# Optimization experiments

Measured on AMD Instinct MI355X. Metric: run time of the kernel, lower is better.

Reference implementation:

```python
import jax, jax.numpy as jnp
import numpy as np

SAMPLE_RATE = 44100
MAX_DURATION = 5.0
IR_LEN = int(SAMPLE_RATE * MAX_DURATION)   # 220500 taps (~5 s reverb tail)
AUDIO_LEN = SAMPLE_RATE * 60               # 60 s of mono audio


def setup_inputs() -> dict:
    key = jax.random.key(0)
    k1, k2 = jax.random.split(key)
    audio = jax.random.normal(k1, (1, AUDIO_LEN), dtype=jnp.float32)
    ir = jax.random.normal(k2, (IR_LEN,), dtype=jnp.float32)  # learned impulse response parameter
    return {"audio": audio, "ir": ir}


def _fft_correlate_valid(audio, ir):
    """Valid cross-correlation of (audio zero-padded by M-1) with ir.

    Matches torch: pad audio with M-1 trailing zeros, then conv1d (which is
    cross-correlation) in 'valid' mode -> output length N. Computed via FFT
    (O(N log N)) instead of direct O(N*M) convolution; identical math up to
    floating-point rounding.
    """
    B, N = audio.shape
    M = ir.shape[0]
    full = (N + M - 1) + M - 1          # full linear conv length of padded signal
    nfft = 1 << int(np.ceil(np.log2(full)))
    # trailing zero-pad covers both the explicit M-1 padding and FFT padding
    x = jnp.pad(audio, ((0, 0), (0, nfft - N)))
    k = jnp.pad(ir[::-1], (0, nfft - M))  # flip kernel: conv(x, flip(ir)) == correlate(x, ir)
    y = jnp.fft.irfft(jnp.fft.rfft(x, axis=-1) * jnp.fft.rfft(k), n=nfft, axis=-1)
    # valid cross-correlation region of the padded signal: indices [M-1, M-1+N)
    return jax.lax.dynamic_slice_in_dim(y, M - 1, N, axis=-1)


def reference(audio, ir):
    y = _fft_correlate_valid(audio, ir)       # [1, N]
    return y / jnp.max(jnp.abs(y))            # global max-abs normalization
```

## Files before the change

### kernel.cpp

```cpp
#include <hip/hip_runtime.h>
#include <hip/hip_fp16.h>


#define L_FFT (1 << 20)
#define GSTRIDE 273
#define PSCALE (1.0f / 1048576.0f)

__device__ __forceinline__ float2 h2f(__half2 h) { return __half22float2(h); }
__device__ __forceinline__ __half2 f2h(float2 v) { return __floats2half2_rn(v.x, v.y); }

__device__ __forceinline__ float2 cmul(float2 a, float2 b) {
    return make_float2(a.x * b.x - a.y * b.y, a.x * b.y + a.y * b.x);
}

__device__ __forceinline__ void rad4(float2 a, float2 b, float2 c, float2 d,
                                     float2& o0, float2& o1, float2& o2, float2& o3) {
    float2 apc = make_float2(a.x + c.x, a.y + c.y);
    float2 amc = make_float2(a.x - c.x, a.y - c.y);
    float2 bpd = make_float2(b.x + d.x, b.y + d.y);
    float2 bmd = make_float2(b.x - d.x, b.y - d.y);
    o0 = make_float2(apc.x + bpd.x, apc.y + bpd.y);
    o2 = make_float2(apc.x - bpd.x, apc.y - bpd.y);
    o1 = make_float2(amc.x + bmd.y, amc.y - bmd.x);
    o3 = make_float2(amc.x - bmd.y, amc.y + bmd.x);
}

__device__ __forceinline__ void dft16(float2 x[16]) {
    float2 tt[16];
    rad4(x[0], x[4], x[8],  x[12], tt[0],  tt[1],  tt[2],  tt[3]);
    rad4(x[1], x[5], x[9],  x[13], tt[4],  tt[5],  tt[6],  tt[7]);
    rad4(x[2], x[6], x[10], x[14], tt[8],  tt[9],  tt[10], tt[11]);
    rad4(x[3], x[7], x[11], x[15], tt[12], tt[13], tt[14], tt[15]);
    const float C1 = 0.92387953251128675613f, S1 = 0.38268343236508977173f;
    const float C2 = 0.70710678118654752440f;
    const float2 W1 = make_float2( C1, -S1);
    const float2 W2 = make_float2( C2, -C2);
    const float2 W3 = make_float2( S1, -C1);
    const float2 W6 = make_float2(-C2, -C2);
    const float2 W9 = make_float2(-C1,  S1);
    tt[5]  = cmul(tt[5],  W1);
    tt[6]  = cmul(tt[6],  W2);
    tt[7]  = cmul(tt[7],  W3);
    tt[9]  = cmul(tt[9],  W2);
    tt[10] = make_float2(tt[10].y, -tt[10].x);
    tt[11] = cmul(tt[11], W6);
    tt[13] = cmul(tt[13], W3);
    tt[14] = cmul(tt[14], W6);
    tt[15] = cmul(tt[15], W9);
    rad4(tt[0], tt[4], tt[8],  tt[12], x[0], x[4], x[8],  x[12]);
    rad4(tt[1], tt[5], tt[9],  tt[13], x[1], x[5], x[9],  x[13]);
    rad4(tt[2], tt[6], tt[10], tt[14], x[2], x[6], x[10], x[14]);
    rad4(tt[3], tt[7], tt[11], tt[15], x[3], x[7], x[11], x[15]);
}

__device__ __forceinline__ void fft256_core(float2 x[16], int i, int gi,
                                            float2* lds) {
    dft16(x);
    float sa, ca;
    __sincosf(-6.28318530717958647692f * (float)i * (1.0f / 256.0f), &sa, &ca);
    float2 w1 = make_float2(ca, sa);
    float2 w = w1;
#pragma unroll
    for (int k1 = 1; k1 < 16; ++k1) {
        x[k1] = cmul(x[k1], w);
        w = cmul(w, w1);
    }
    float2* base = lds + gi * GSTRIDE;
#pragma unroll
    for (int k1 = 0; k1 < 16; ++k1) base[i * 17 + k1] = x[k1];
    __syncthreads();
#pragma unroll
    for (int q1 = 0; q1 < 16; ++q1) x[q1] = base[q1 * 17 + i];
    dft16(x);
}

__device__ __forceinline__ void fft4096_block(float2 x[16], int tid, float2* lds) {
    dft16(x);
    float sa, ca;
    __sincosf(-6.28318530717958647692f * (float)tid * (1.0f / 4096.0f), &sa, &ca);
    float2 w1 = make_float2(ca, sa);
    float2 w = w1;
#pragma unroll
    for (int a = 1; a < 16; ++a) { x[a] = cmul(x[a], w); w = cmul(w, w1); }
#pragma unroll
    for (int a = 0; a < 16; ++a) lds[a * GSTRIDE + tid] = x[a];
    __syncthreads();
    int an = tid & 15, i2 = tid >> 4;
#pragma unroll
    for (int q = 0; q < 16; ++q) x[q] = lds[an * GSTRIDE + i2 + 16 * q];
    __syncthreads();
    fft256_core(x, i2, an, lds);
}

__device__ __forceinline__ void fft4096_pair(float2 x[16], float2 h[16], int tid,
                                             float2* LX, float2* LH) {
    dft16(x);
    dft16(h);
    float sa, ca;
    __sincosf(-6.28318530717958647692f * (float)tid * (1.0f / 4096.0f), &sa, &ca);
    float2 w1 = make_float2(ca, sa);
    float2 w = w1;
#pragma unroll
    for (int a = 1; a < 16; ++a) {
        x[a] = cmul(x[a], w);
        h[a] = cmul(h[a], w);
        w = cmul(w, w1);
    }
#pragma unroll
    for (int a = 0; a < 16; ++a) {
        LX[a * GSTRIDE + tid] = x[a];
        LH[a * GSTRIDE + tid] = h[a];
    }
    __syncthreads();
    int an = tid & 15, i2 = tid >> 4;
#pragma unroll
    for (int q = 0; q < 16; ++q) {
        x[q] = LX[an * GSTRIDE + i2 + 16 * q];
        h[q] = LH[an * GSTRIDE + i2 + 16 * q];
    }
    __syncthreads();
    fft256_core(x, i2, an, LX);
    fft256_core(h, i2, an, LH);
}

__global__ void fwd1_pack(const float* __restrict__ audio,
                          const float* __restrict__ ir,
                          __half2* __restrict__ dst, int N, int M, int V) {
    __shared__ float2 lds[16 * GSTRIDE];
    int tid = threadIdx.x;
    int gi = tid & 15, i = tid >> 4;
    int bx = blockIdx.x, slot = blockIdx.y;
    int g = bx * 16 + gi;
    __half2* db = dst + (size_t)slot * L_FFT;

    float2 x[16];
#pragma unroll
    for (int q2 = 0; q2 < 16; ++q2) {
        int idx = g + (i + 16 * q2) * (L_FFT / 256);
        float2 v;
        if (slot == 0) {
            v = make_float2(audio[idx], audio[idx + V]);
        } else if (slot == 1) {
            float a2 = (idx + 2 * V < N) ? audio[idx + 2 * V] : 0.f;
            float a3 = (idx + 3 * V < N) ? audio[idx + 3 * V] : 0.f;
            v = make_float2(a2, a3);
        } else {
            v = make_float2((idx < M) ? ir[idx] : 0.f, 0.f);
        }
        x[q2] = v;
    }
    fft256_core(x, i, gi, lds);
    float sa, ca;
    float base = -6.28318530717958647692f * (float)g * (1.0f / (float)L_FFT);
    __sincosf(base * (float)i, &sa, &ca);
    float2 w = make_float2(ca, sa);
    __sincosf(base * 16.0f, &sa, &ca);
    float2 w16 = make_float2(ca, sa);
#pragma unroll
    for (int q = 0; q < 16; ++q) {
        db[(size_t)4096 * (i + 16 * q) + g] = f2h(cmul(x[q], w));
        w = cmul(w, w16);
    }
}

__global__ __launch_bounds__(256, 2) void fused_mid(const __half2* __restrict__ Y1,
                                                    __half2* __restrict__ Mp) {
    __shared__ float2 LX[16 * GSTRIDE];
    __shared__ float2 LH[16 * GSTRIDE];
    int tid = threadIdx.x;
    int b0 = blockIdx.x, p = blockIdx.y;
    const __half2* xr = Y1 + (size_t)p * L_FFT + (size_t)4096 * b0;
    const __half2* hr = Y1 + (size_t)2 * L_FFT + (size_t)4096 * b0;
    float2 x[16], h[16];
#pragma unroll
    for (int w = 0; w < 16; ++w) {
        x[w] = h2f(xr[tid + 256 * w]);
        h[w] = h2f(hr[tid + 256 * w]);
    }
    fft4096_pair(x, h, tid, LX, LH);
#pragma unroll
    for (int r = 0; r < 16; ++r) {
        float2 Z = x[r], H = h[r];
        x[r] = make_float2((Z.x * H.x + Z.y * H.y) * PSCALE,
                           (Z.x * H.y - Z.y * H.x) * PSCALE);
    }
    fft4096_block(x, tid, LX);
    float sa, ca;
    float base = -6.28318530717958647692f * (float)b0 * (1.0f / (float)L_FFT);
    __sincosf(base * (float)tid, &sa, &ca);
    float2 w = make_float2(ca, sa);
    __sincosf(base * 256.0f, &sa, &ca);
    float2 ws = make_float2(ca, sa);
    __half2* dst = Mp + (size_t)p * L_FFT + (size_t)4096 * b0;
#pragma unroll
    for (int r = 0; r < 16; ++r) {
        dst[tid + 256 * r] = f2h(cmul(x[r], w));
        w = cmul(w, ws);
    }
}

__global__ void inv_max(const __half2* __restrict__ Mp,
                        float* __restrict__ partials, int N, int V) {
    __shared__ float2 lds[16 * GSTRIDE];
    int tid = threadIdx.x;
    int gi = tid & 15, i = tid >> 4;
    int bx = blockIdx.x, p = blockIdx.y;
    const __half2* sb = Mp + (size_t)p * L_FFT;
    int na = 16 * bx + gi;
    float2 x[16];
#pragma unroll
    for (int q = 0; q < 16; ++q)
        x[q] = h2f(sb[(size_t)4096 * (i + 16 * q) + na]);
    fft256_core(x, i, gi, lds);
    int nbase = na + 4096 * i;
    int lenO = (p == 1) ? (N - 3 * V) : V;
    float m = 0.f;
#pragma unroll
    for (int r = 0; r < 16; ++r) {
        int n = nbase + r * 65536;
        if (n < V)    m = fmaxf(m, fabsf(x[r].x));
        if (n < lenO) m = fmaxf(m, fabsf(x[r].y));
    }
    for (int o = 32; o > 0; o >>= 1) m = fmaxf(m, __shfl_xor(m, o));
    __shared__ float sm[4];
    int lane = tid & 63, wv = tid >> 6;
    if (lane == 0) sm[wv] = m;
    __syncthreads();
    if (tid == 0)
        partials[blockIdx.y * gridDim.x + blockIdx.x] =
            fmaxf(fmaxf(sm[0], sm[1]), fmaxf(sm[2], sm[3]));
}

__global__ void norm_write(const __half2* __restrict__ Mp,
                           float* __restrict__ out,
                           const float* __restrict__ partials, int N, int V) {
    __shared__ float2 lds[16 * GSTRIDE];
    __shared__ float sm[4];
    int tid = threadIdx.x;
    int gi = tid & 15, i = tid >> 4;
    int bx = blockIdx.x, p = blockIdx.y;
    const __half2* sb = Mp + (size_t)p * L_FFT;
    int na = 16 * bx + gi;
    float2 x[16];
#pragma unroll
    for (int q = 0; q < 16; ++q)
        x[q] = h2f(sb[(size_t)4096 * (i + 16 * q) + na]);

    float m = 0.f;
    for (int t = tid; t < 512; t += 256) m = fmaxf(m, partials[t]);
    for (int o = 32; o > 0; o >>= 1) m = fmaxf(m, __shfl_xor(m, o));
    int lane = tid & 63, wv = tid >> 6;
    if (lane == 0) sm[wv] = m;
    __syncthreads();
    float inv = 1.0f / fmaxf(fmaxf(sm[0], sm[1]), fmaxf(sm[2], sm[3]));

    fft256_core(x, i, gi, lds);
    int nbase = na + 4096 * i;
    int se = 2 * p, so = 2 * p + 1;
    int lenO = (p == 1) ? (N - 3 * V) : V;
#pragma unroll
    for (int r = 0; r < 16; ++r) {
        int n = nbase + r * 65536;
        if (n < V)    out[(size_t)se * V + n] = x[r].x * inv;
        if (n < lenO) out[(size_t)so * V + n] = -x[r].y * inv;
    }
}

extern "C" void kernel_launch(void* const* d_in, const int* in_sizes, int n_in,
                              void* d_out, int out_size, void* d_ws, size_t ws_size,
                              hipStream_t stream) {
    const float* audio = (const float*)d_in[0];
    const float* ir    = (const float*)d_in[1];
    float* out = (float*)d_out;

    const int N = in_sizes[0];
    const int M = in_sizes[1];
    const int V = L_FFT - M + 1;

    __half2* A = (__half2*)d_ws;
    __half2* B = A + (size_t)3 * L_FFT;
    float* partials = (float*)(B + (size_t)3 * L_FFT);

    fwd1_pack<<<dim3(256, 3), 256, 0, stream>>>(audio, ir, B, N, M, V);
    fused_mid<<<dim3(256, 2), 256, 0, stream>>>(B, A);
    inv_max<<<dim3(256, 2), 256, 0, stream>>>(A, partials, N, V);
    norm_write<<<dim3(256, 2), 256, 0, stream>>>(A, out, partials, N, V);
}
```

Before: 101.4 us.

## Fuse inverse FFT max and normalize write via grid-wide atomic barrier

Merges the inv_max and norm_write kernels into one kernel that keeps the inverse-FFT results in registers. Blocks publish their max through atomicMax on the float bits, then spin on an arrival counter until all 512 blocks are done before scaling and writing output. This removes a kernel launch, a second read of the spectrum and a second 256-point FFT pass. It relies on all 512 blocks being co-resident (launch_bounds 256,2 on 256 CUs) and could deadlock if they are not.

```diff
diff --git a/kernel.cpp b/kernel.cpp
--- a/kernel.cpp
+++ b/kernel.cpp
@@ -5,6 +5,7 @@
 #define L_FFT (1 << 20)
 #define GSTRIDE 273
 #define PSCALE (1.0f / 1048576.0f)
+#define NBLK_INV 512
 
 __device__ __forceinline__ float2 h2f(__half2 h) { return __half22float2(h); }
 __device__ __forceinline__ __half2 f2h(float2 v) { return __floats2half2_rn(v.x, v.y); }
@@ -164,11 +165,13 @@
 }
 
 __global__ __launch_bounds__(256, 2) void fused_mid(const __half2* __restrict__ Y1,
-                                                    __half2* __restrict__ Mp) {
+                                                    __half2* __restrict__ Mp,
+                                                    unsigned* __restrict__ sync2) {
     __shared__ float2 LX[16 * GSTRIDE];
     __shared__ float2 LH[16 * GSTRIDE];
     int tid = threadIdx.x;
     int b0 = blockIdx.x, p = blockIdx.y;
+    if (b0 == 0 && p == 0 && tid == 0) { sync2[0] = 0u; sync2[1] = 0u; }
     const __half2* xr = Y1 + (size_t)p * L_FFT + (size_t)4096 * b0;
     const __half2* hr = Y1 + (size_t)2 * L_FFT + (size_t)4096 * b0;
     float2 x[16], h[16];
@@ -199,9 +202,12 @@
     }
 }
 
-__global__ void inv_max(const __half2* __restrict__ Mp,
-                        float* __restrict__ partials, int N, int V) {
+__global__ __launch_bounds__(256, 2) void inv_norm_write(
+        const __half2* __restrict__ Mp, float* __restrict__ out,
+        unsigned* __restrict__ sync2, int N, int V) {
     __shared__ float2 lds[16 * GSTRIDE];
+    __shared__ float sm[4];
+    __shared__ float bcast;
     int tid = threadIdx.x;
     int gi = tid & 15, i = tid >> 4;
     int bx = blockIdx.x, p = blockIdx.y;
@@ -222,42 +228,24 @@
         if (n < lenO) m = fmaxf(m, fabsf(x[r].y));
     }
     for (int o = 32; o > 0; o >>= 1) m = fmaxf(m, __shfl_xor(m, o));
-    __shared__ float sm[4];
     int lane = tid & 63, wv = tid >> 6;
     if (lane == 0) sm[wv] = m;
     __syncthreads();
-    if (tid == 0)
-        partials[blockIdx.y * gridDim.x + blockIdx.x] =
-            fmaxf(fmaxf(sm[0], sm[1]), fmaxf(sm[2], sm[3]));
-}
-
-__global__ void norm_write(const __half2* __restrict__ Mp,
-                           float* __restrict__ out,
-                           const float* __restrict__ partials, int N, int V) {
-    __shared__ float2 lds[16 * GSTRIDE];
-    __shared__ float sm[4];
-    int tid = threadIdx.x;
-    int gi = tid & 15, i = tid >> 4;
-    int bx = blockIdx.x, p = blockIdx.y;
-    const __half2* sb = Mp + (size_t)p * L_FFT;
-    int na = 16 * bx + gi;
-    float2 x[16];
-#pragma unroll
-    for (int q = 0; q < 16; ++q)
-        x[q] = h2f(sb[(size_t)4096 * (i + 16 * q) + na]);
-
-    float m = 0.f;
-    for (int t = tid; t < 512; t += 256) m = fmaxf(m, partials[t]);
-    for (int o = 32; o > 0; o >>= 1) m = fmaxf(m, __shfl_xor(m, o));
-    int lane = tid & 63, wv = tid >> 6;
-    if (lane == 0) sm[wv] = m;
-    __syncthreads();
-    float inv = 1.0f / fmaxf(fmaxf(sm[0], sm[1]), fmaxf(sm[2], sm[3]));
-
-    fft256_core(x, i, gi, lds);
-    int nbase = na + 4096 * i;
+    if (tid == 0) {
+        float bm = fmaxf(fmaxf(sm[0], sm[1]), fmaxf(sm[2], sm[3]));
+        atomicMax(&sync2[0], __float_as_uint(bm));
+        __threadfence();
+        atomicAdd(&sync2[1], 1u);
+        while (__hip_atomic_load(&sync2[1], __ATOMIC_ACQUIRE,
+                                 __HIP_MEMORY_SCOPE_AGENT) < NBLK_INV) {
+            __builtin_amdgcn_s_sleep(1);
+        }
+        bcast = __uint_as_float(__hip_atomic_load(&sync2[0], __ATOMIC_ACQUIRE,
+                                                  __HIP_MEMORY_SCOPE_AGENT));
+    }
+    __syncthreads();
+    float inv = 1.0f / bcast;
     int se = 2 * p, so = 2 * p + 1;
-    int lenO = (p == 1) ? (N - 3 * V) : V;
 #pragma unroll
     for (int r = 0; r < 16; ++r) {
         int n = nbase + r * 65536;
@@ -279,10 +267,9 @@
 
     __half2* A = (__half2*)d_ws;
     __half2* B = A + (size_t)3 * L_FFT;
-    float* partials = (float*)(B + (size_t)3 * L_FFT);
+    unsigned* sync2 = (unsigned*)(B + (size_t)3 * L_FFT);
 
     fwd1_pack<<<dim3(256, 3), 256, 0, stream>>>(audio, ir, B, N, M, V);
-    fused_mid<<<dim3(256, 2), 256, 0, stream>>>(B, A);
-    inv_max<<<dim3(256, 2), 256, 0, stream>>>(A, partials, N, V);
-    norm_write<<<dim3(256, 2), 256, 0, stream>>>(A, out, partials, N, V);
-}
+    fused_mid<<<dim3(256, 2), 256, 0, stream>>>(B, A, sync2);
+    inv_norm_write<<<dim3(256, 2), 256, 0, stream>>>(A, out, sync2, N, V);
+}
```

Result: slower. 134.5 us (+32.7%).
